# Kernel optimization log

Measured on AMD Instinct MI355X. Metric: run time of the kernel, lower is better.

Reference implementation:

```python
import jax, jax.numpy as jnp
import numpy as np

B, T, D_IN, H1, H2 = 32, 2048, 1024, 512, 32


def setup_inputs() -> dict:
    key = jax.random.key(0)
    ks = jax.random.split(key, 8)
    avf_out = jax.random.normal(ks[0], (B, T, D_IN), dtype=jnp.float32)
    # seq_len in [1, T] so every sample has a non-empty slice (matches torch usage)
    seq_len = jax.random.randint(ks[1], (B,), 1, T + 1, dtype=jnp.int32)
    s = 0.02
    W1 = jax.random.normal(ks[2], (D_IN, H1), dtype=jnp.float32) * s
    b1 = jnp.zeros((H1,), dtype=jnp.float32)
    W2 = jax.random.normal(ks[3], (H1, H2), dtype=jnp.float32) * s
    b2 = jnp.zeros((H2,), dtype=jnp.float32)
    W3 = jax.random.normal(ks[4], (H2, 1), dtype=jnp.float32) * s
    b3 = jnp.zeros((1,), dtype=jnp.float32)
    return {"avf_out": avf_out, "W1": W1, "b1": b1, "W2": W2, "b2": b2,
            "W3": W3, "b3": b3, "seq_len": seq_len}


def reference(avf_out, W1, b1, W2, b2, W3, b3, seq_len):
    h = jax.nn.relu(jnp.einsum('btd,dh->bth', avf_out, W1) + b1)
    h = jnp.einsum('bth,hk->btk', h, W2) + b2
    logits = jax.nn.sigmoid(jnp.einsum('btk,ko->bto', h, W3) + b3)[..., 0]  # [B, T]
    # ragged per-sample top-k (k = seq_len//16 + 1 over first seq_len entries) + mean,
    # vectorized via masked descending sort + cumsum (no per-sample loop)
    Tn = logits.shape[1]
    valid = jnp.arange(Tn)[None, :] < seq_len[:, None]            # [B, T]
    NEG = jnp.float32(-1.0)  # below sigmoid range, so padded slots never enter top-k
    masked = jnp.where(valid, logits, NEG)
    sorted_desc = -jnp.sort(-masked, axis=1)                      # [B, T] descending
    csum = jnp.cumsum(sorted_desc, axis=1)
    k = seq_len // 16 + 1                                         # k <= seq_len always
    topk_sum = jnp.take_along_axis(csum, (k - 1)[:, None].astype(jnp.int32), axis=1)[:, 0]
    return topk_sum / k.astype(logits.dtype)                      # [B]
```

## Files before the change

kernel.cpp:

```cpp
#include <hip/hip_runtime.h>

typedef __bf16 bf16;
typedef __bf16 bf16x4 __attribute__((ext_vector_type(4)));
typedef __bf16 bf16x8 __attribute__((ext_vector_type(8)));
typedef float f32x4 __attribute__((ext_vector_type(4)));

#define K_TOT 1024
#define N_TOT 512
#define T_SEQ 2048
#define NB 32

__device__ __forceinline__ void async16(const void* g, void* l) {
    __builtin_amdgcn_global_load_lds(
        (const __attribute__((address_space(1))) unsigned int*)g,
        (__attribute__((address_space(3))) unsigned int*)l, 16, 0, 0);
}

__global__ __launch_bounds__(256) void transpose_w1(const float* __restrict__ W1,
                                                    bf16* __restrict__ W1T) {
    __shared__ float tile[32][33];
    const int t = threadIdx.x;
    const int k0 = blockIdx.x * 32;
    const int n0 = blockIdx.y * 32;
#pragma unroll
    for (int p = 0; p < 4; p++) {
        int kl = p * 8 + (t >> 5);
        int nl = t & 31;
        tile[kl][nl] = W1[(k0 + kl) * 512 + n0 + nl];
    }
    __syncthreads();
#pragma unroll
    for (int p = 0; p < 4; p++) {
        int nl = p * 8 + (t >> 5);
        int kl = t & 31;
        W1T[(n0 + nl) * 1024 + k0 + kl] = (bf16)tile[kl][nl];
    }
}

__global__ __launch_bounds__(512) void prep(const float* __restrict__ W2,
                                            const float* __restrict__ b2,
                                            const float* __restrict__ W3,
                                            const float* __restrict__ b3,
                                            const int* __restrict__ seq_len,
                                            float* __restrict__ v,
                                            int* __restrict__ tiles) {
    const int t = threadIdx.x;
    float s = 0.f;
#pragma unroll
    for (int c = 0; c < 32; c++) s += W2[t * 32 + c] * W3[c];
    v[t] = s;
    if (t == 0) {
        float cc = b3[0];
        for (int c = 0; c < 32; c++) cc += b2[c] * W3[c];
        v[512] = cc;
    }
    __shared__ int nb[32], off[32];
    if (t < 32) nb[t] = (seq_len[t] + 127) >> 7;
    __syncthreads();
    if (t == 0) {
        int a = 0;
        for (int i = 0; i < 32; i++) { off[i] = a; a += nb[i]; }
        tiles[0] = a;
    }
    __syncthreads();
    const int b = t >> 4, j = t & 15;
    if (j < nb[b]) tiles[1 + off[b] + j] = t;
}

__device__ __forceinline__ int sw_idx(int row, int e) {
    return row * 64 + (((e >> 3) ^ (row & 7)) << 3) + (e & 7);
}

__global__ __launch_bounds__(512, 2) void gemm_fused(const float* __restrict__ A,
                                                     const bf16* __restrict__ W1T,
                                                     const float* __restrict__ b1,
                                                     const float* __restrict__ v,
                                                     const int* __restrict__ tiles,
                                                     float* __restrict__ logits) {
    __shared__ bf16 smem[2][(128 + 512) * 64];

    const int nact = tiles[0];
    if ((int)blockIdx.x >= nact) return;
    const int m0 = tiles[1 + blockIdx.x] * 128;

    const int t = threadIdx.x;
    const int wave = t >> 6, lane = t & 63;
    const int q = lane >> 4, l15 = lane & 15;
    const int wm = wave >> 2, wn = wave & 3;

    const int arow = t >> 2, ac = t & 3;
    const float* agp = A + (size_t)(m0 + arow) * K_TOT + ac * 4;

    const int bl_row = wave * 64 + (lane >> 3);
    const int bl_chunk = (lane & 7) ^ ((lane >> 3) & 7);
    const bf16* bgp = W1T + (size_t)bl_row * K_TOT + bl_chunk * 8;

    f32x4 acc[4][8] = {};
    float4 av[4];

    auto loadA = [&](int k0) {
#pragma unroll
        for (int p = 0; p < 4; p++) av[p] = *(const float4*)(agp + k0 + p * 16);
    };
    auto asyncB = [&](int k0, int b) {
        bf16* bs = smem[b] + 128 * 64;
#pragma unroll
        for (int j = 0; j < 8; j++)
            async16(bgp + k0 + (size_t)j * 8 * K_TOT, bs + (wave * 64 + j * 8) * 64);
    };
    auto writeA = [&](int b) {
        bf16* as = smem[b];
#pragma unroll
        for (int p = 0; p < 4; p++) {
            bf16x4 w;
            w[0] = (bf16)av[p].x; w[1] = (bf16)av[p].y;
            w[2] = (bf16)av[p].z; w[3] = (bf16)av[p].w;
            int chunk = 2 * p + (ac >> 1);
            int idx = arow * 64 + ((chunk ^ (arow & 7)) << 3) + (ac & 1) * 4;
            *(bf16x4*)(&as[idx]) = w;
        }
    };
    auto mfma_phase = [&](int b) {
        const bf16* as = smem[b];
        const bf16* bs = smem[b] + 128 * 64;
#pragma unroll
        for (int kk = 0; kk < 64; kk += 32) {
            const int e = kk + q * 8;
            bf16x8 af[4], bfv[8];
#pragma unroll
            for (int mi = 0; mi < 4; mi++)
                af[mi] = *(const bf16x8*)(&as[sw_idx(wm * 64 + mi * 16 + l15, e)]);
#pragma unroll
            for (int ni = 0; ni < 8; ni++)
                bfv[ni] = *(const bf16x8*)(&bs[sw_idx(wn * 128 + ni * 16 + l15, e)]);
#pragma unroll
            for (int mi = 0; mi < 4; mi++)
#pragma unroll
                for (int ni = 0; ni < 8; ni++)
                    acc[mi][ni] = __builtin_amdgcn_mfma_f32_16x16x32_bf16(
                        af[mi], bfv[ni], acc[mi][ni], 0, 0, 0);
        }
    };

    loadA(0);
    asyncB(0, 0);
    writeA(0);
    __syncthreads();

#pragma unroll 1
    for (int k = 0; k < 16; k++) {
        const int buf = k & 1, nxt = buf ^ 1;
        if (k < 15) {
            loadA((k + 1) * 64);
            asyncB((k + 1) * 64, nxt);
        }
        mfma_phase(buf);
        if (k < 15) writeA(nxt);
        __syncthreads();
    }

    float bb[8], vv[8];
#pragma unroll
    for (int ni = 0; ni < 8; ni++) {
        int col = wn * 128 + ni * 16 + l15;
        bb[ni] = b1[col];
        vv[ni] = v[col];
    }
    const float cconst = v[512];

    __syncthreads();
    float* part = (float*)smem;

#pragma unroll
    for (int mi = 0; mi < 4; mi++) {
#pragma unroll
        for (int r = 0; r < 4; r++) {
            float s = 0.f;
#pragma unroll
            for (int ni = 0; ni < 8; ni++)
                s += fmaxf(acc[mi][ni][r] + bb[ni], 0.f) * vv[ni];
            s += __shfl_xor(s, 1);
            s += __shfl_xor(s, 2);
            s += __shfl_xor(s, 4);
            s += __shfl_xor(s, 8);
            if (l15 == 0) {
                int row = wm * 64 + mi * 16 + q * 4 + r;
                part[row * 4 + wn] = s;
            }
        }
    }
    __syncthreads();
    if (t < 128) {
        float s = part[t * 4] + part[t * 4 + 1] + part[t * 4 + 2] + part[t * 4 + 3] + cconst;
        logits[m0 + t] = 1.f / (1.f + __expf(-s));
    }
}

__global__ __launch_bounds__(256) void topk_mean(const float* __restrict__ logits,
                                                 const int* __restrict__ seq_len,
                                                 float* __restrict__ out) {
    __shared__ float vals[T_SEQ];
    __shared__ int redi[4];
    __shared__ float redf[4];
    const int b = blockIdx.x, t = threadIdx.x;
    const int lane = t & 63, wave = t >> 6;
    const int L = seq_len[b];
    const int k = (L >> 4) + 1;
    const float* p = logits + b * T_SEQ;
    for (int i = t; i < L; i += 256) vals[i] = p[i];
    __syncthreads();

    unsigned lo = 0u, hi = 0x3f800000u;
    while (lo < hi) {
        unsigned mid = lo + ((hi - lo + 1) >> 1);
        float thr = __uint_as_float(mid);
        int cnt = 0;
        for (int i = t; i < L; i += 256) cnt += (vals[i] >= thr) ? 1 : 0;
#pragma unroll
        for (int m = 32; m >= 1; m >>= 1) cnt += __shfl_xor(cnt, m);
        if (lane == 0) redi[wave] = cnt;
        __syncthreads();
        int total = redi[0] + redi[1] + redi[2] + redi[3];
        __syncthreads();
        if (total >= k) lo = mid; else hi = mid - 1;
    }
    const float thr = __uint_as_float(lo);

    int cnt = 0; float sum = 0.f;
    for (int i = t; i < L; i += 256) {
        float x = vals[i];
        if (x > thr) { cnt += 1; sum += x; }
    }
#pragma unroll
    for (int m = 32; m >= 1; m >>= 1) { cnt += __shfl_xor(cnt, m); sum += __shfl_xor(sum, m); }
    if (lane == 0) { redi[wave] = cnt; redf[wave] = sum; }
    __syncthreads();
    if (t == 0) {
        int cgt = redi[0] + redi[1] + redi[2] + redi[3];
        float sgt = redf[0] + redf[1] + redf[2] + redf[3];
        out[b] = (sgt + (float)(k - cgt) * thr) / (float)k;
    }
}

extern "C" void kernel_launch(void* const* d_in, const int* in_sizes, int n_in,
                              void* d_out, int out_size, void* d_ws, size_t ws_size,
                              hipStream_t stream) {
    const float* avf = (const float*)d_in[0];
    const float* W1  = (const float*)d_in[1];
    const float* b1  = (const float*)d_in[2];
    const float* W2  = (const float*)d_in[3];
    const float* b2  = (const float*)d_in[4];
    const float* W3  = (const float*)d_in[5];
    const float* b3  = (const float*)d_in[6];
    const int* seq_len = (const int*)d_in[7];
    float* out = (float*)d_out;

    char* ws = (char*)d_ws;
    bf16*  W1T    = (bf16*)ws;
    float* v      = (float*)(ws + (1 << 20));
    int*   tiles  = (int*)(ws + (1 << 20) + 4096);
    float* logits = (float*)(ws + (1 << 20) + 8192);

    transpose_w1<<<dim3(32, 16), 256, 0, stream>>>(W1, W1T);
    prep<<<1, 512, 0, stream>>>(W2, b2, W3, b3, seq_len, v, tiles);
    gemm_fused<<<512, 512, 0, stream>>>(avf, W1T, b1, v, tiles, logits);
    topk_mean<<<NB, 256, 0, stream>>>(logits, seq_len, out);
}
```

Baseline: 417.8 us.

## Fuse prep into transpose and top-k into GEMM via last-block atomic counter

Merges the prep kernel into the W1 transpose kernel and folds the per-sample top-k mean into the GEMM kernel, so four launches become two. The last GEMM block to finish each sample, found through an atomic counter with threadfences, does the threshold search on the logits. The search now starts from the observed min/max and tests two thresholds per pass (ternary) with packed counts, which cuts the number of barrier-bound reduction rounds. The cost is that the final selection runs serially at the tail of whichever block finishes last, and correctness now depends on memory fences and on resetting the counter in every run.

Result: no change. 411.6 us (-1.5%).

```diff
diff --git a/kernel.cpp b/kernel.cpp
--- a/kernel.cpp
+++ b/kernel.cpp
@@ -16,9 +16,14 @@
         (__attribute__((address_space(3))) unsigned int*)l, 16, 0, 0);
 }
 
-__global__ __launch_bounds__(256) void transpose_w1(const float* __restrict__ W1,
-                                                    bf16* __restrict__ W1T) {
+__global__ __launch_bounds__(256) void transpose_prep(
+        const float* __restrict__ W1, bf16* __restrict__ W1T,
+        const float* __restrict__ W2, const float* __restrict__ b2,
+        const float* __restrict__ W3, const float* __restrict__ b3,
+        const int* __restrict__ seq_len,
+        float* __restrict__ v, int* __restrict__ tiles, int* __restrict__ done) {
     __shared__ float tile[32][33];
+    __shared__ int nb2[32], off2[32];
     const int t = threadIdx.x;
     const int k0 = blockIdx.x * 32;
     const int n0 = blockIdx.y * 32;
@@ -35,36 +40,35 @@
         int kl = t & 31;
         W1T[(n0 + nl) * 1024 + k0 + kl] = (bf16)tile[kl][nl];
     }
-}
-
-__global__ __launch_bounds__(512) void prep(const float* __restrict__ W2,
-                                            const float* __restrict__ b2,
-                                            const float* __restrict__ W3,
-                                            const float* __restrict__ b3,
-                                            const int* __restrict__ seq_len,
-                                            float* __restrict__ v,
-                                            int* __restrict__ tiles) {
-    const int t = threadIdx.x;
-    float s = 0.f;
-#pragma unroll
-    for (int c = 0; c < 32; c++) s += W2[t * 32 + c] * W3[c];
-    v[t] = s;
-    if (t == 0) {
-        float cc = b3[0];
-        for (int c = 0; c < 32; c++) cc += b2[c] * W3[c];
-        v[512] = cc;
-    }
-    __shared__ int nb[32], off[32];
-    if (t < 32) nb[t] = (seq_len[t] + 127) >> 7;
-    __syncthreads();
-    if (t == 0) {
-        int a = 0;
-        for (int i = 0; i < 32; i++) { off[i] = a; a += nb[i]; }
-        tiles[0] = a;
-    }
-    __syncthreads();
-    const int b = t >> 4, j = t & 15;
-    if (j < nb[b]) tiles[1 + off[b] + j] = t;
+
+    if (blockIdx.x == 0 && blockIdx.y == 0) {
+        for (int h = t; h < 512; h += 256) {
+            float s = 0.f;
+#pragma unroll
+            for (int c = 0; c < 32; c++) s += W2[h * 32 + c] * W3[c];
+            v[h] = s;
+        }
+        if (t == 0) {
+            float cc = b3[0];
+            for (int c = 0; c < 32; c++) cc += b2[c] * W3[c];
+            v[512] = cc;
+        }
+        if (t < 32) {
+            nb2[t] = (seq_len[t] + 127) >> 7;
+            done[t] = 0;
+        }
+        __syncthreads();
+        if (t == 0) {
+            int a = 0;
+            for (int i = 0; i < 32; i++) { off2[i] = a; a += nb2[i]; }
+            tiles[0] = a;
+        }
+        __syncthreads();
+        for (int idx = t; idx < 512; idx += 256) {
+            int b = idx >> 4, j = idx & 15;
+            if (j < nb2[b]) tiles[1 + off2[b] + j] = idx;
+        }
+    }
 }
 
 __device__ __forceinline__ int sw_idx(int row, int e) {
@@ -76,12 +80,17 @@
                                                      const float* __restrict__ b1,
                                                      const float* __restrict__ v,
                                                      const int* __restrict__ tiles,
-                                                     float* __restrict__ logits) {
+                                                     const int* __restrict__ seq_len,
+                                                     int* __restrict__ done,
+                                                     float* __restrict__ logits,
+                                                     float* __restrict__ out) {
     __shared__ bf16 smem[2][(128 + 512) * 64];
 
     const int nact = tiles[0];
     if ((int)blockIdx.x >= nact) return;
-    const int m0 = tiles[1 + blockIdx.x] * 128;
+    const int tileid = tiles[1 + blockIdx.x];
+    const int m0 = tileid * 128;
+    const int bsmp = tileid >> 4;
 
     const int t = threadIdx.x;
     const int wave = t >> 6, lane = t & 63;
@@ -194,51 +203,98 @@
         float s = part[t * 4] + part[t * 4 + 1] + part[t * 4 + 2] + part[t * 4 + 3] + cconst;
         logits[m0 + t] = 1.f / (1.f + __expf(-s));
     }
-}
-
-__global__ __launch_bounds__(256) void topk_mean(const float* __restrict__ logits,
-                                                 const int* __restrict__ seq_len,
-                                                 float* __restrict__ out) {
-    __shared__ float vals[T_SEQ];
-    __shared__ int redi[4];
-    __shared__ float redf[4];
-    const int b = blockIdx.x, t = threadIdx.x;
-    const int lane = t & 63, wave = t >> 6;
-    const int L = seq_len[b];
-    const int k = (L >> 4) + 1;
-    const float* p = logits + b * T_SEQ;
-    for (int i = t; i < L; i += 256) vals[i] = p[i];
-    __syncthreads();
-
-    unsigned lo = 0u, hi = 0x3f800000u;
+
+    const int L = seq_len[bsmp];
+    const int nb = (L + 127) >> 7;
+
+    float* vals  = (float*)smem;
+    int*   redi  = (int*)(vals + 2048);
+    unsigned* mnx = (unsigned*)(redi + 16);
+    float* redf  = (float*)(mnx + 16);
+    int*   wflag = (int*)(redf + 8);
+
+    __syncthreads();
+    if (t == 0) {
+        __threadfence();
+        int old = atomicAdd(&done[bsmp], 1);
+        int win = (old == nb - 1);
+        if (win) __threadfence();
+        *wflag = win;
+    }
+    __syncthreads();
+    if (!*wflag) return;
+
+    const int kk = (L >> 4) + 1;
+    const float* p = logits + bsmp * T_SEQ;
+
+    unsigned mn = 0x3f800000u, mx = 0u;
+    for (int i = t; i < L; i += 512) {
+        float x = p[i];
+        vals[i] = x;
+        unsigned u = __float_as_uint(x);
+        mn = min(mn, u); mx = max(mx, u);
+    }
+#pragma unroll
+    for (int m = 32; m >= 1; m >>= 1) {
+        mn = min(mn, (unsigned)__shfl_xor((int)mn, m));
+        mx = max(mx, (unsigned)__shfl_xor((int)mx, m));
+    }
+    if (lane == 0) { mnx[wave] = mn; mnx[8 + wave] = mx; }
+    __syncthreads();
+    unsigned lo = mnx[0], hi = mnx[8];
+#pragma unroll
+    for (int w8 = 1; w8 < 8; w8++) {
+        lo = min(lo, mnx[w8]); hi = max(hi, mnx[8 + w8]);
+    }
+    __syncthreads();
+
+    int rb = 0;
     while (lo < hi) {
-        unsigned mid = lo + ((hi - lo + 1) >> 1);
-        float thr = __uint_as_float(mid);
-        int cnt = 0;
-        for (int i = t; i < L; i += 256) cnt += (vals[i] >= thr) ? 1 : 0;
-#pragma unroll
-        for (int m = 32; m >= 1; m >>= 1) cnt += __shfl_xor(cnt, m);
-        if (lane == 0) redi[wave] = cnt;
+        unsigned w = hi - lo;
+        unsigned t1 = w / 3u + 1u;
+        unsigned m1 = lo + t1;
+        unsigned m2 = lo + (w - w / 3u);
+        if (m2 < m1) m2 = m1;
+        float f1 = __uint_as_float(m1), f2 = __uint_as_float(m2);
+        int c1 = 0, c2 = 0;
+        for (int i = t; i < L; i += 512) {
+            float x = vals[i];
+            c1 += (x >= f1) ? 1 : 0;
+            c2 += (x >= f2) ? 1 : 0;
+        }
+        int packed = (c1 << 12) | c2;
+#pragma unroll
+        for (int m = 32; m >= 1; m >>= 1) packed += __shfl_xor(packed, m);
+        if (lane == 0) redi[(rb & 1) * 8 + wave] = packed;
         __syncthreads();
-        int total = redi[0] + redi[1] + redi[2] + redi[3];
-        __syncthreads();
-        if (total >= k) lo = mid; else hi = mid - 1;
+        int tot = 0;
+#pragma unroll
+        for (int w8 = 0; w8 < 8; w8++) tot += redi[(rb & 1) * 8 + w8];
+        int C2 = tot & 0xFFF, C1 = tot >> 12;
+        if (C2 >= kk)      { lo = m2; }
+        else if (C1 >= kk) { lo = m1; hi = m2 - 1; }
+        else               { hi = m1 - 1; }
+        rb++;
     }
     const float thr = __uint_as_float(lo);
 
-    int cnt = 0; float sum = 0.f;
-    for (int i = t; i < L; i += 256) {
+    int cg = 0; float sg = 0.f;
+    for (int i = t; i < L; i += 512) {
         float x = vals[i];
-        if (x > thr) { cnt += 1; sum += x; }
-    }
-#pragma unroll
-    for (int m = 32; m >= 1; m >>= 1) { cnt += __shfl_xor(cnt, m); sum += __shfl_xor(sum, m); }
-    if (lane == 0) { redi[wave] = cnt; redf[wave] = sum; }
+        if (x > thr) { cg += 1; sg += x; }
+    }
+#pragma unroll
+    for (int m = 32; m >= 1; m >>= 1) {
+        cg += __shfl_xor(cg, m);
+        sg += __shfl_xor(sg, m);
+    }
+    if (lane == 0) { redi[(rb & 1) * 8 + wave] = cg; redf[wave] = sg; }
     __syncthreads();
     if (t == 0) {
-        int cgt = redi[0] + redi[1] + redi[2] + redi[3];
-        float sgt = redf[0] + redf[1] + redf[2] + redf[3];
-        out[b] = (sgt + (float)(k - cgt) * thr) / (float)k;
+        int cgt = 0; float sgt = 0.f;
+#pragma unroll
+        for (int w8 = 0; w8 < 8; w8++) { cgt += redi[(rb & 1) * 8 + w8]; sgt += redf[w8]; }
+        out[bsmp] = (sgt + (float)(kk - cgt) * thr) / (float)kk;
     }
 }
 
@@ -259,10 +315,11 @@
     bf16*  W1T    = (bf16*)ws;
     float* v      = (float*)(ws + (1 << 20));
     int*   tiles  = (int*)(ws + (1 << 20) + 4096);
-    float* logits = (float*)(ws + (1 << 20) + 8192);
-
-    transpose_w1<<<dim3(32, 16), 256, 0, stream>>>(W1, W1T);
-    prep<<<1, 512, 0, stream>>>(W2, b2, W3, b3, seq_len, v, tiles);
-    gemm_fused<<<512, 512, 0, stream>>>(avf, W1T, b1, v, tiles, logits);
-    topk_mean<<<NB, 256, 0, stream>>>(logits, seq_len, out);
-}
+    int*   done   = (int*)(ws + (1 << 20) + 8192);
+    float* logits = (float*)(ws + (1 << 20) + 12288);
+
+    transpose_prep<<<dim3(32, 16), 256, 0, stream>>>(W1, W1T, W2, b2, W3, b3,
+                                                     seq_len, v, tiles, done);
+    gemm_fused<<<512, 512, 0, stream>>>(avf, W1T, b1, v, tiles, seq_len, done,
+                                        logits, out);
+}
```
